# Optimization experiments

Measured on AMD Instinct MI355X. Metric: run time of the kernel, lower is better.

The kernel has to match this reference:

```python
import jax, jax.numpy as jnp
import numpy as np


def _next_fast_len(n):
    # smallest 5-smooth integer >= n (matches scipy.fftpack.next_fast_len)
    while True:
        m = n
        for p in (2, 3, 5):
            while m % p == 0:
                m //= p
        if m == 1:
            return n
        n += 1


def _conv1d_fft(values, weights):
    # values: [b, h, n, d], weights: [h, m]; FFT cross-correlation implementing
    # causal exponentially-decaying weighted sum (per-head EMA of values).
    N = values.shape[-2]
    M = weights.shape[-1]
    L = _next_fast_len(N + M - 1)
    f_v = jnp.fft.rfft(values, n=L, axis=-2)          # [b,h,F,d] complex
    f_w = jnp.fft.rfft(weights, n=L, axis=-1)         # [h,F]   complex
    out = jnp.fft.irfft(f_v * jnp.conj(f_w)[..., None], n=L, axis=-2)
    out = jnp.roll(out, -1, axis=-2)
    return out[..., L - N:, :]                         # [b,h,N,d]


def setup_inputs() -> dict:
    key = jax.random.key(0)
    ks = jax.random.split(key, 7)
    B, N, D, H = 4, 8192, 512, 8
    s = 1.0 / np.sqrt(D)
    return {
        "x": jax.random.normal(ks[0], (B, N, D), dtype=jnp.float32),
        "W_in": jax.random.normal(ks[1], (D, D), dtype=jnp.float32) * s,
        "b_in": jax.random.normal(ks[2], (D,), dtype=jnp.float32) * 0.01,
        "W_out": jax.random.normal(ks[3], (D, D), dtype=jnp.float32) * s,
        "b_out": jax.random.normal(ks[4], (D,), dtype=jnp.float32) * 0.01,
        "init_state": jax.random.normal(ks[5], (H, D // H), dtype=jnp.float32),
        "alpha_param": jax.random.normal(ks[6], (H,), dtype=jnp.float32),
    }


def reference(x, W_in, b_in, W_out, b_out, init_state, alpha_param):
    B, N, D = x.shape
    H, Dh = init_state.shape
    # input projection
    xp = x @ W_in.T + b_in                             # [B,N,D]
    xh = xp.reshape(B, N, H, Dh).transpose(0, 2, 1, 3)  # [B,H,N,Dh]
    # prepend learned init state, take first differences along time
    x0 = jnp.broadcast_to(init_state[None, :, None, :], (B, H, 1, Dh))
    xc = jnp.concatenate([x0, xh], axis=2)             # [B,H,N+1,Dh]
    xd = xc[:, :, 1:] - xc[:, :, :-1]                  # [B,H,N,Dh]
    # per-head smoothing coefficients
    alpha = jax.nn.sigmoid(alpha_param)[:, None]       # [H,1]
    ar = jnp.arange(N, dtype=x.dtype)
    weights = alpha * (1.0 - alpha) ** ar[::-1]        # [H,N]
    out = _conv1d_fft(xd, weights)                     # [B,H,N,Dh]
    # contribution of the initial state
    init_w = (1.0 - alpha) ** (ar + 1.0)               # [H,N]
    out = out + init_w[:, :, None] * init_state[:, None, :]
    out = out.transpose(0, 2, 1, 3).reshape(B, N, D)
    return out @ W_out.T + b_out
```

## Files before the change

kernel.cpp:

```cpp
#include <hip/hip_runtime.h>
#include <stdint.h>

#define SEQ      8192
#define BATCH    4
#define DIM      512
#define MROWS    32768
#define CHUNK    64
#define NCHUNK   128
#define NCHAN    2048

typedef unsigned short ushort;
typedef unsigned int   uint;
typedef __bf16 bf16x8 __attribute__((ext_vector_type(8)));
typedef float  f32x4  __attribute__((ext_vector_type(4)));
typedef ushort usx8   __attribute__((ext_vector_type(8)));

__device__ __forceinline__ ushort f2bf(float f) {
    unsigned u = __float_as_uint(f);
    unsigned r = (u + 0x7fffu + ((u >> 16) & 1u)) >> 16;
    return (ushort)r;
}
__device__ __forceinline__ float bf2f(ushort v) {
    return __uint_as_float(((unsigned)v) << 16);
}

__global__ void weights_to_bf16_kernel(const float* __restrict__ w_in,
                                       const float* __restrict__ w_out,
                                       ushort* __restrict__ dst, int n4each) {
    int i = blockIdx.x * blockDim.x + threadIdx.x;
    if (i >= 2 * n4each) return;
    const float4* src = (i < n4each) ? (const float4*)w_in
                                     : (const float4*)w_out - n4each;
    float4 v = src[i];
    ushort4 r;
    r.x = f2bf(v.x); r.y = f2bf(v.y); r.z = f2bf(v.z); r.w = f2bf(v.w);
    ((ushort4*)dst)[i] = r;
}

#define GLDS(g, l) __builtin_amdgcn_global_load_lds(                        \
        (const __attribute__((address_space(1))) void*)(g),                 \
        (__attribute__((address_space(3))) void*)(l), 16, 0, 0)

template <bool A_F32, bool OUT_BF16>
__global__ __launch_bounds__(512, 4) void gemm_kernel(
        const void* __restrict__ Aptr, const ushort* __restrict__ Bw,
        const float* __restrict__ bias, void* __restrict__ Cout,
        int M, int N, int K)
{
    __shared__ __align__(16) ushort As[2][128 * 32];
    __shared__ __align__(16) ushort Bs[2][256 * 32];

    const int tid  = threadIdx.x;
    const int lane = tid & 63;
    const int wave = tid >> 6;
    const int wr = wave >> 2, wc = wave & 3;
    const int bm = blockIdx.y, bn = blockIdx.x;
    const int quad = lane >> 4, r16 = lane & 15;

    const int srow = tid >> 2;
    const int skoff = (tid & 3) * 8;
    const float*  Ag32 = (const float*) Aptr + (size_t)(bm * 128 + srow) * K + skoff;
    const ushort* Ag16 = (const ushort*)Aptr + (size_t)(bm * 128 + srow) * K + skoff;
    const ushort* Bg0 = Bw + (size_t)(bn * 256 + srow) * K + skoff;
    const ushort* Bg1 = Bg0 + (size_t)128 * K;

    f32x4 acc[4][4];
    #pragma unroll
    for (int i = 0; i < 4; i++)
        #pragma unroll
        for (int j = 0; j < 4; j++)
            acc[i][j] = f32x4{0.f, 0.f, 0.f, 0.f};

    const int nIter = K / 32;

    auto stageB = [&](int k0, int b) {
        GLDS(Bg0 + k0, &Bs[b][tid * 8]);
        GLDS(Bg1 + k0, &Bs[b][128 * 32 + tid * 8]);
    };
    auto stageA16 = [&](int k0, int b) {
        GLDS(Ag16 + k0, &As[b][tid * 8]);
    };

    stageB(0, 0);
    float a0[8];
    if (A_F32) {
        #pragma unroll
        for (int u = 0; u < 8; u++) a0[u] = Ag32[u];
        usx8 w;
        #pragma unroll
        for (int u = 0; u < 8; u++) w[u] = f2bf(a0[u]);
        *(usx8*)&As[0][tid * 8] = w;
    } else {
        stageA16(0, 0);
    }

    int buf = 0;
    for (int k = 0; k < nIter; ++k) {
        __syncthreads();

        float anext[8];
        const bool more = (k + 1 < nIter);
        if (more) {
            const int ko = (k + 1) * 32;
            stageB(ko, buf ^ 1);
            if (A_F32) {
                #pragma unroll
                for (int u = 0; u < 8; u++) anext[u] = Ag32[ko + u];
            } else {
                stageA16(ko, buf ^ 1);
            }
        }

        bf16x8 af[4], bfr[4];
        #pragma unroll
        for (int i = 0; i < 4; i++)
            af[i] = *(const bf16x8*)&As[buf][(wr * 64 + i * 16 + r16) * 32 + quad * 8];
        #pragma unroll
        for (int j = 0; j < 4; j++)
            bfr[j] = *(const bf16x8*)&Bs[buf][(wc * 64 + j * 16 + r16) * 32 + quad * 8];

        #pragma unroll
        for (int i = 0; i < 4; i++)
            #pragma unroll
            for (int j = 0; j < 4; j++)
                acc[i][j] = __builtin_amdgcn_mfma_f32_16x16x32_bf16(
                                bfr[j], af[i], acc[i][j], 0, 0, 0);

        if (A_F32 && more) {
            usx8 w;
            #pragma unroll
            for (int u = 0; u < 8; u++) w[u] = f2bf(anext[u]);
            *(usx8*)&As[buf ^ 1][tid * 8] = w;
        }
        buf ^= 1;
    }

    #pragma unroll
    for (int i = 0; i < 4; i++) {
        const int m = bm * 128 + wr * 64 + i * 16 + r16;
        #pragma unroll
        for (int j = 0; j < 4; j++) {
            const int n0 = bn * 256 + wc * 64 + j * 16 + quad * 4;
            const float4 bv = *(const float4*)&bias[n0];
            float v0 = acc[i][j][0] + bv.x;
            float v1 = acc[i][j][1] + bv.y;
            float v2 = acc[i][j][2] + bv.z;
            float v3 = acc[i][j][3] + bv.w;
            size_t idx = (size_t)m * N + n0;
            if (OUT_BF16) {
                ushort4 r;
                r.x = f2bf(v0); r.y = f2bf(v1); r.z = f2bf(v2); r.w = f2bf(v3);
                *(ushort4*)&((ushort*)Cout)[idx] = r;
            } else {
                *(float4*)&((float*)Cout)[idx] = make_float4(v0, v1, v2, v3);
            }
        }
    }
}

template <bool WRITE_Z>
__global__ void scan_kernel(const ushort* __restrict__ xp,
                            const float* __restrict__ alpha_param,
                            const float* __restrict__ init_state,
                            const float* __restrict__ Zin,
                            float* __restrict__ Lfin,
                            ushort* __restrict__ zout)
{
    const int tid   = threadIdx.x;
    const int chunk = blockIdx.x;
    const int b     = blockIdx.y;
    const int d0    = tid * 2;
    const int h     = d0 >> 6;

    const float alpha = 1.0f / (1.0f + expf(-alpha_param[h]));
    const float cdec  = 1.0f - alpha;
    const int   t0    = chunk * CHUNK;
    const size_t baseRow = (size_t)b * SEQ;
    const int ch0 = b * DIM + d0;

    float prev0, prev1;
    if (chunk == 0) {
        prev0 = init_state[d0]; prev1 = init_state[d0 + 1];
    } else {
        uint u = *(const uint*)&xp[(baseRow + t0 - 1) * DIM + d0];
        prev0 = bf2f((ushort)(u & 0xffffu)); prev1 = bf2f((ushort)(u >> 16));
    }
    float z0 = 0.f, z1 = 0.f;
    if (WRITE_Z) {
        z0 = Zin[(size_t)ch0 * NCHUNK + chunk];
        z1 = Zin[(size_t)(ch0 + 1) * NCHUNK + chunk];
    }

    const ushort* p = xp + (baseRow + t0) * DIM + d0;
    ushort* q = WRITE_Z ? (zout + (baseRow + t0) * DIM + d0) : nullptr;
    #pragma unroll 8
    for (int t = 0; t < CHUNK; ++t) {
        uint u = *(const uint*)&p[(size_t)t * DIM];
        float cur0 = bf2f((ushort)(u & 0xffffu));
        float cur1 = bf2f((ushort)(u >> 16));
        z0 = cdec * z0 + alpha * (cur0 - prev0);
        z1 = cdec * z1 + alpha * (cur1 - prev1);
        prev0 = cur0; prev1 = cur1;
        if (WRITE_Z) {
            uint w = (uint)f2bf(z0) | ((uint)f2bf(z1) << 16);
            *(uint*)&q[(size_t)t * DIM] = w;
        }
    }
    if (!WRITE_Z) {
        Lfin[(size_t)ch0 * NCHUNK + chunk]       = z0;
        Lfin[(size_t)(ch0 + 1) * NCHUNK + chunk] = z1;
    }
}

__global__ void scan_fix_kernel(const float* __restrict__ Lfin,
                                const float* __restrict__ alpha_param,
                                const float* __restrict__ init_state,
                                float* __restrict__ Zin)
{
    int ch = blockIdx.x * blockDim.x + threadIdx.x;
    if (ch >= NCHAN) return;
    int d = ch & (DIM - 1);
    int h = d >> 6;
    float alpha = 1.0f / (1.0f + expf(-alpha_param[h]));
    float c = 1.0f - alpha;
    float cT = c;
    #pragma unroll
    for (int i = 0; i < 6; i++) cT *= cT;
    float Z = init_state[d];
    const float* L = Lfin + (size_t)ch * NCHUNK;
    float*      Zp = Zin  + (size_t)ch * NCHUNK;
    for (int i = 0; i < NCHUNK; i++) { Zp[i] = Z; Z = L[i] + cT * Z; }
}

extern "C" void kernel_launch(void* const* d_in, const int* in_sizes, int n_in,
                              void* d_out, int out_size, void* d_ws, size_t ws_size,
                              hipStream_t stream) {
    const float* x           = (const float*)d_in[0];
    const float* W_in        = (const float*)d_in[1];
    const float* b_in        = (const float*)d_in[2];
    const float* W_out       = (const float*)d_in[3];
    const float* b_out       = (const float*)d_in[4];
    const float* init_state  = (const float*)d_in[5];
    const float* alpha_param = (const float*)d_in[6];
    float* out = (float*)d_out;

    ushort* z_bf    = (ushort*)d_ws;
    ushort* win_bf  = z_bf   + (size_t)MROWS * DIM;
    ushort* wout_bf = win_bf + (size_t)DIM * DIM;
    ushort* xp_bf   = wout_bf + (size_t)DIM * DIM;
    float*  Lfin    = (float*)(xp_bf + (size_t)MROWS * DIM);
    float*  Zin     = Lfin + (size_t)NCHAN * NCHUNK;

    const int nw4 = (DIM * DIM) / 4;
    weights_to_bf16_kernel<<<(2 * nw4 + 255) / 256, 256, 0, stream>>>(
        W_in, W_out, win_bf, nw4);

    dim3 ggrid(DIM / 256, MROWS / 128);
    gemm_kernel<true, true><<<ggrid, 512, 0, stream>>>(
        (const void*)x, win_bf, b_in, (void*)xp_bf, MROWS, DIM, DIM);

    dim3 sgrid(NCHUNK, BATCH);
    scan_kernel<false><<<sgrid, 256, 0, stream>>>(
        xp_bf, alpha_param, init_state, nullptr, Lfin, nullptr);
    scan_fix_kernel<<<NCHAN / 256, 256, 0, stream>>>(
        Lfin, alpha_param, init_state, Zin);
    scan_kernel<true><<<sgrid, 256, 0, stream>>>(
        xp_bf, alpha_param, init_state, Zin, nullptr, z_bf);

    gemm_kernel<false, false><<<ggrid, 512, 0, stream>>>(
        (const void*)z_bf, wout_bf, b_out, (void*)out, MROWS, DIM, DIM);
}
```

Measured before the change: 212.8 us.

## Fuse chunk carry-in correction into output GEMM, dropping second scan pass

The local scan now writes chunk-local EMA results straight to the z buffer and emits chunk-final states in a chunk-major layout. The carry fix-up kernel reads that transposed layout with register prefetching. The second full scan pass over xp is removed: the output GEMM's A-loader adds the (1-alpha)^(tau+1)·Zin carry term while staging each tile. This saves a full read of xp and a full write of z, at the cost of extra ALU and Zin loads in the GEMM loader. It also adds one more bf16 rounding of the corrected value.

```diff
diff --git a/kernel.cpp b/kernel.cpp
--- a/kernel.cpp
+++ b/kernel.cpp
@@ -8,6 +8,7 @@
 #define CHUNK    64
 #define NCHUNK   128
 #define NCHAN    2048
+#define NHEAD    8
 
 typedef unsigned short ushort;
 typedef unsigned int   uint;
@@ -41,10 +42,11 @@
         (const __attribute__((address_space(1))) void*)(g),                 \
         (__attribute__((address_space(3))) void*)(l), 16, 0, 0)
 
-template <bool A_F32, bool OUT_BF16>
+template <int AMODE, bool OUT_BF16>
 __global__ __launch_bounds__(512, 4) void gemm_kernel(
         const void* __restrict__ Aptr, const ushort* __restrict__ Bw,
         const float* __restrict__ bias, void* __restrict__ Cout,
+        const float* __restrict__ Zin, const float* __restrict__ alpha_param,
         int M, int N, int K)
 {
     __shared__ __align__(16) ushort As[2][128 * 32];
@@ -63,6 +65,54 @@
     const ushort* Ag16 = (const ushort*)Aptr + (size_t)(bm * 128 + srow) * K + skoff;
     const ushort* Bg0 = Bw + (size_t)(bn * 256 + srow) * K + skoff;
     const ushort* Bg1 = Bg0 + (size_t)128 * K;
+
+    float fc0=0.f,fc1=0.f,fc2=0.f,fc3=0.f,fc4=0.f,fc5=0.f,fc6=0.f,fc7=0.f;
+    const float* Zc = nullptr;
+    if (AMODE == 2) {
+        const int m   = bm * 128 + srow;
+        const int tau = m & (CHUNK - 1);
+        const int bb  = m >> 13;
+        const int tch = (m & (SEQ - 1)) >> 6;
+        Zc = Zin + (size_t)tch * NCHAN + (size_t)bb * DIM;
+        const float t1 = (float)(tau + 1);
+        float a, c;
+        a = 1.f/(1.f+expf(-alpha_param[0])); c = 1.f - a; fc0 = exp2f(t1 * log2f(c));
+        a = 1.f/(1.f+expf(-alpha_param[1])); c = 1.f - a; fc1 = exp2f(t1 * log2f(c));
+        a = 1.f/(1.f+expf(-alpha_param[2])); c = 1.f - a; fc2 = exp2f(t1 * log2f(c));
+        a = 1.f/(1.f+expf(-alpha_param[3])); c = 1.f - a; fc3 = exp2f(t1 * log2f(c));
+        a = 1.f/(1.f+expf(-alpha_param[4])); c = 1.f - a; fc4 = exp2f(t1 * log2f(c));
+        a = 1.f/(1.f+expf(-alpha_param[5])); c = 1.f - a; fc5 = exp2f(t1 * log2f(c));
+        a = 1.f/(1.f+expf(-alpha_param[6])); c = 1.f - a; fc6 = exp2f(t1 * log2f(c));
+        a = 1.f/(1.f+expf(-alpha_param[7])); c = 1.f - a; fc7 = exp2f(t1 * log2f(c));
+    }
+    auto selfac = [&](int hh) -> float {
+        float f = fc0;
+        f = (hh == 1) ? fc1 : f;
+        f = (hh == 2) ? fc2 : f;
+        f = (hh == 3) ? fc3 : f;
+        f = (hh == 4) ? fc4 : f;
+        f = (hh == 5) ? fc5 : f;
+        f = (hh == 6) ? fc6 : f;
+        f = (hh == 7) ? fc7 : f;
+        return f;
+    };
+    auto stageA2 = [&](int ko, int b) {
+        usx8 av = *(const usx8*)(Ag16 + ko);
+        const int dbase = ko + skoff;
+        float4 zv0 = *(const float4*)&Zc[dbase];
+        float4 zv1 = *(const float4*)&Zc[dbase + 4];
+        float fac = selfac(dbase >> 6);
+        usx8 w;
+        w[0] = f2bf(bf2f(av[0]) + fac * zv0.x);
+        w[1] = f2bf(bf2f(av[1]) + fac * zv0.y);
+        w[2] = f2bf(bf2f(av[2]) + fac * zv0.z);
+        w[3] = f2bf(bf2f(av[3]) + fac * zv0.w);
+        w[4] = f2bf(bf2f(av[4]) + fac * zv1.x);
+        w[5] = f2bf(bf2f(av[5]) + fac * zv1.y);
+        w[6] = f2bf(bf2f(av[6]) + fac * zv1.z);
+        w[7] = f2bf(bf2f(av[7]) + fac * zv1.w);
+        *(usx8*)&As[b][tid * 8] = w;
+    };
 
     f32x4 acc[4][4];
     #pragma unroll
@@ -82,14 +132,16 @@
     };
 
     stageB(0, 0);
-    float a0[8];
-    if (A_F32) {
+    if (AMODE == 1) {
+        float a0[8];
         #pragma unroll
         for (int u = 0; u < 8; u++) a0[u] = Ag32[u];
         usx8 w;
         #pragma unroll
         for (int u = 0; u < 8; u++) w[u] = f2bf(a0[u]);
         *(usx8*)&As[0][tid * 8] = w;
+    } else if (AMODE == 2) {
+        stageA2(0, 0);
     } else {
         stageA16(0, 0);
     }
@@ -99,13 +151,20 @@
         __syncthreads();
 
         float anext[8];
+        usx8 av_n; float4 zn0, zn1; float fac_n = 0.f;
         const bool more = (k + 1 < nIter);
         if (more) {
             const int ko = (k + 1) * 32;
             stageB(ko, buf ^ 1);
-            if (A_F32) {
+            if (AMODE == 1) {
                 #pragma unroll
                 for (int u = 0; u < 8; u++) anext[u] = Ag32[ko + u];
+            } else if (AMODE == 2) {
+                av_n = *(const usx8*)(Ag16 + ko);
+                const int dbase = ko + skoff;
+                zn0 = *(const float4*)&Zc[dbase];
+                zn1 = *(const float4*)&Zc[dbase + 4];
+                fac_n = selfac(dbase >> 6);
             } else {
                 stageA16(ko, buf ^ 1);
             }
@@ -126,11 +185,24 @@
                 acc[i][j] = __builtin_amdgcn_mfma_f32_16x16x32_bf16(
                                 bfr[j], af[i], acc[i][j], 0, 0, 0);
 
-        if (A_F32 && more) {
-            usx8 w;
-            #pragma unroll
-            for (int u = 0; u < 8; u++) w[u] = f2bf(anext[u]);
-            *(usx8*)&As[buf ^ 1][tid * 8] = w;
+        if (more) {
+            if (AMODE == 1) {
+                usx8 w;
+                #pragma unroll
+                for (int u = 0; u < 8; u++) w[u] = f2bf(anext[u]);
+                *(usx8*)&As[buf ^ 1][tid * 8] = w;
+            } else if (AMODE == 2) {
+                usx8 w;
+                w[0] = f2bf(bf2f(av_n[0]) + fac_n * zn0.x);
+                w[1] = f2bf(bf2f(av_n[1]) + fac_n * zn0.y);
+                w[2] = f2bf(bf2f(av_n[2]) + fac_n * zn0.z);
+                w[3] = f2bf(bf2f(av_n[3]) + fac_n * zn0.w);
+                w[4] = f2bf(bf2f(av_n[4]) + fac_n * zn1.x);
+                w[5] = f2bf(bf2f(av_n[5]) + fac_n * zn1.y);
+                w[6] = f2bf(bf2f(av_n[6]) + fac_n * zn1.z);
+                w[7] = f2bf(bf2f(av_n[7]) + fac_n * zn1.w);
+                *(usx8*)&As[buf ^ 1][tid * 8] = w;
+            }
         }
         buf ^= 1;
     }
@@ -158,13 +230,11 @@
     }
 }
 
-template <bool WRITE_Z>
-__global__ void scan_kernel(const ushort* __restrict__ xp,
-                            const float* __restrict__ alpha_param,
-                            const float* __restrict__ init_state,
-                            const float* __restrict__ Zin,
-                            float* __restrict__ Lfin,
-                            ushort* __restrict__ zout)
+__global__ void scan_local_kernel(const ushort* __restrict__ xp,
+                                  const float* __restrict__ alpha_param,
+                                  const float* __restrict__ init_state,
+                                  float* __restrict__ Lfin,
+                                  ushort* __restrict__ zout)
 {
     const int tid   = threadIdx.x;
     const int chunk = blockIdx.x;
@@ -186,13 +256,8 @@
         prev0 = bf2f((ushort)(u & 0xffffu)); prev1 = bf2f((ushort)(u >> 16));
     }
     float z0 = 0.f, z1 = 0.f;
-    if (WRITE_Z) {
-        z0 = Zin[(size_t)ch0 * NCHUNK + chunk];
-        z1 = Zin[(size_t)(ch0 + 1) * NCHUNK + chunk];
-    }
-
-    const ushort* p = xp + (baseRow + t0) * DIM + d0;
-    ushort* q = WRITE_Z ? (zout + (baseRow + t0) * DIM + d0) : nullptr;
+    const ushort* p = xp   + (baseRow + t0) * DIM + d0;
+    ushort*       q = zout + (baseRow + t0) * DIM + d0;
     #pragma unroll 8
     for (int t = 0; t < CHUNK; ++t) {
         uint u = *(const uint*)&p[(size_t)t * DIM];
@@ -201,21 +266,16 @@
         z0 = cdec * z0 + alpha * (cur0 - prev0);
         z1 = cdec * z1 + alpha * (cur1 - prev1);
         prev0 = cur0; prev1 = cur1;
-        if (WRITE_Z) {
-            uint w = (uint)f2bf(z0) | ((uint)f2bf(z1) << 16);
-            *(uint*)&q[(size_t)t * DIM] = w;
-        }
-    }
-    if (!WRITE_Z) {
-        Lfin[(size_t)ch0 * NCHUNK + chunk]       = z0;
-        Lfin[(size_t)(ch0 + 1) * NCHUNK + chunk] = z1;
-    }
-}
-
-__global__ void scan_fix_kernel(const float* __restrict__ Lfin,
-                                const float* __restrict__ alpha_param,
-                                const float* __restrict__ init_state,
-                                float* __restrict__ Zin)
+        uint w = (uint)f2bf(z0) | ((uint)f2bf(z1) << 16);
+        *(uint*)&q[(size_t)t * DIM] = w;
+    }
+    *(float2*)&Lfin[(size_t)chunk * NCHAN + ch0] = make_float2(z0, z1);
+}
+
+__global__ void scan_fix2_kernel(const float* __restrict__ Lfin,
+                                 const float* __restrict__ alpha_param,
+                                 const float* __restrict__ init_state,
+                                 float* __restrict__ Zin)
 {
     int ch = blockIdx.x * blockDim.x + threadIdx.x;
     if (ch >= NCHAN) return;
@@ -227,9 +287,22 @@
     #pragma unroll
     for (int i = 0; i < 6; i++) cT *= cT;
     float Z = init_state[d];
-    const float* L = Lfin + (size_t)ch * NCHUNK;
-    float*      Zp = Zin  + (size_t)ch * NCHUNK;
-    for (int i = 0; i < NCHUNK; i++) { Zp[i] = Z; Z = L[i] + cT * Z; }
+    const float* Lp = Lfin + ch;
+    float*       Zp = Zin  + ch;
+    constexpr int PF = 16;
+    float Lr[PF];
+    #pragma unroll
+    for (int j = 0; j < PF; ++j) Lr[j] = Lp[(size_t)j * NCHAN];
+    for (int g = 0; g < NCHUNK / PF; ++g) {
+        #pragma unroll
+        for (int j = 0; j < PF; ++j) {
+            float Lc = Lr[j];
+            if (g + 1 < NCHUNK / PF)
+                Lr[j] = Lp[(size_t)((g + 1) * PF + j) * NCHAN];
+            Zp[(size_t)(g * PF + j) * NCHAN] = Z;
+            Z = Lc + cT * Z;
+        }
+    }
 }
 
 extern "C" void kernel_launch(void* const* d_in, const int* in_sizes, int n_in,
@@ -256,17 +329,17 @@
         W_in, W_out, win_bf, nw4);
 
     dim3 ggrid(DIM / 256, MROWS / 128);
-    gemm_kernel<true, true><<<ggrid, 512, 0, stream>>>(
-        (const void*)x, win_bf, b_in, (void*)xp_bf, MROWS, DIM, DIM);
+    gemm_kernel<1, true><<<ggrid, 512, 0, stream>>>(
+        (const void*)x, win_bf, b_in, (void*)xp_bf,
+        nullptr, nullptr, MROWS, DIM, DIM);
 
     dim3 sgrid(NCHUNK, BATCH);
-    scan_kernel<false><<<sgrid, 256, 0, stream>>>(
-        xp_bf, alpha_param, init_state, nullptr, Lfin, nullptr);
-    scan_fix_kernel<<<NCHAN / 256, 256, 0, stream>>>(
+    scan_local_kernel<<<sgrid, 256, 0, stream>>>(
+        xp_bf, alpha_param, init_state, Lfin, z_bf);
+    scan_fix2_kernel<<<NCHAN / 256, 256, 0, stream>>>(
         Lfin, alpha_param, init_state, Zin);
-    scan_kernel<true><<<sgrid, 256, 0, stream>>>(
-        xp_bf, alpha_param, init_state, Zin, nullptr, z_bf);
-
-    gemm_kernel<false, false><<<ggrid, 512, 0, stream>>>(
-        (const void*)z_bf, wout_bf, b_out, (void*)out, MROWS, DIM, DIM);
-}
+
+    gemm_kernel<2, false><<<ggrid, 512, 0, stream>>>(
+        (const void*)z_bf, wout_bf, b_out, (void*)out,
+        Zin, alpha_param, MROWS, DIM, DIM);
+}
```

Result: faster. 208.5 us (-2.0%).

## Fuse input GEMM with chunk-local scan and apply carry correction in output GEMM

Applied to the files above, without the earlier changes.

The input projection GEMM now runs the per-chunk EMA scan in its epilogue from a shared-memory tile. It writes chunk-local z and chunk summaries directly, which removes the xp round trip through global memory and both scan passes. A small fix-up kernel computes per-chunk carries. The output GEMM folds the decayed carry into its A operand as it loads it into shared memory. W_in is converted to bf16 inline, and W_out conversion is packed into extra blocks of the first kernel. The cost is extra in-loop f32 conversion and pow work in the GEMMs, and z is rounded to bf16 before the correction is added.

```diff
diff --git a/kernel.cpp b/kernel.cpp
--- a/kernel.cpp
+++ b/kernel.cpp
@@ -8,6 +8,9 @@
 #define CHUNK    64
 #define NCHUNK   128
 #define NCHAN    2048
+#define NHEAD    8
+#define NGCHUNK  512
+#define XLD      264
 
 typedef unsigned short ushort;
 typedef unsigned int   uint;
@@ -24,28 +27,206 @@
     return __uint_as_float(((unsigned)v) << 16);
 }
 
-__global__ void weights_to_bf16_kernel(const float* __restrict__ w_in,
-                                       const float* __restrict__ w_out,
-                                       ushort* __restrict__ dst, int n4each) {
-    int i = blockIdx.x * blockDim.x + threadIdx.x;
-    if (i >= 2 * n4each) return;
-    const float4* src = (i < n4each) ? (const float4*)w_in
-                                     : (const float4*)w_out - n4each;
-    float4 v = src[i];
-    ushort4 r;
-    r.x = f2bf(v.x); r.y = f2bf(v.y); r.z = f2bf(v.z); r.w = f2bf(v.w);
-    ((ushort4*)dst)[i] = r;
+__global__ __launch_bounds__(512, 4) void gemm1_scan_kernel(
+        const float* __restrict__ x,    const float* __restrict__ W_in,
+        const float* __restrict__ b_in, const float* __restrict__ W_out,
+        const float* __restrict__ alpha_param,
+        ushort* __restrict__ zout,      ushort* __restrict__ wout_bf,
+        float* __restrict__ Lfin,       float* __restrict__ XpT)
+{
+    const int tid = threadIdx.x;
+    const int bn  = blockIdx.x;
+
+    if (blockIdx.y == 0) {
+        const float4* src = (const float4*)W_out;
+        const int n4 = (DIM * DIM) / 4;
+        for (int idx = bn * 512 + tid; idx < n4; idx += 1024) {
+            float4 v = src[idx];
+            ushort4 r;
+            r.x = f2bf(v.x); r.y = f2bf(v.y); r.z = f2bf(v.z); r.w = f2bf(v.w);
+            ((ushort4*)wout_bf)[idx] = r;
+        }
+        return;
+    }
+    const int bm = blockIdx.y - 1;
+
+    __shared__ __align__(16) char smem[2 * XLD * 128];
+    ushort* As0 = (ushort*)smem;
+    ushort* Bs0 = (ushort*)(smem + 16384);
+    ushort* X   = (ushort*)smem;
+
+    const int lane = tid & 63;
+    const int wave = tid >> 6;
+    const int wr = wave >> 2, wc = wave & 3;
+    const int quad = lane >> 4, r16 = lane & 15;
+
+    const int srow  = tid >> 2;
+    const int skoff = (tid & 3) * 8;
+    const float* Ag  = x    + (size_t)(bm * 128 + srow) * DIM + skoff;
+    const float* Bg0 = W_in + (size_t)(bn * 256 + srow) * DIM + skoff;
+    const float* Bg1 = Bg0  + (size_t)128 * DIM;
+
+    f32x4 acc[4][4];
+    #pragma unroll
+    for (int i = 0; i < 4; i++)
+        #pragma unroll
+        for (int j = 0; j < 4; j++)
+            acc[i][j] = f32x4{0.f, 0.f, 0.f, 0.f};
+
+    const int nIter = DIM / 32;
+
+    auto cvt8 = [&](const float* s) {
+        usx8 w;
+        #pragma unroll
+        for (int u = 0; u < 8; u++) w[u] = f2bf(s[u]);
+        return w;
+    };
+
+    {
+        float a[8], b0[8], b1[8];
+        #pragma unroll
+        for (int u = 0; u < 8; u++) { a[u] = Ag[u]; b0[u] = Bg0[u]; b1[u] = Bg1[u]; }
+        *(usx8*)&As0[tid * 8]        = cvt8(a);
+        *(usx8*)&Bs0[tid * 8]        = cvt8(b0);
+        *(usx8*)&Bs0[4096 + tid * 8] = cvt8(b1);
+    }
+
+    int buf = 0;
+    for (int k = 0; k < nIter; ++k) {
+        __syncthreads();
+
+        float an[8], bn0[8], bn1[8];
+        const bool more = (k + 1 < nIter);
+        if (more) {
+            const int ko = (k + 1) * 32;
+            #pragma unroll
+            for (int u = 0; u < 8; u++) {
+                an[u]  = Ag[ko + u];
+                bn0[u] = Bg0[ko + u];
+                bn1[u] = Bg1[ko + u];
+            }
+        }
+
+        bf16x8 af[4], bfr[4];
+        #pragma unroll
+        for (int i = 0; i < 4; i++)
+            af[i] = *(const bf16x8*)&As0[buf * 4096 + (wr * 64 + i * 16 + r16) * 32 + quad * 8];
+        #pragma unroll
+        for (int j = 0; j < 4; j++)
+            bfr[j] = *(const bf16x8*)&Bs0[buf * 8192 + (wc * 64 + j * 16 + r16) * 32 + quad * 8];
+
+        #pragma unroll
+        for (int i = 0; i < 4; i++)
+            #pragma unroll
+            for (int j = 0; j < 4; j++)
+                acc[i][j] = __builtin_amdgcn_mfma_f32_16x16x32_bf16(
+                                bfr[j], af[i], acc[i][j], 0, 0, 0);
+
+        if (more) {
+            const int nb = buf ^ 1;
+            *(usx8*)&As0[nb * 4096 + tid * 8]        = cvt8(an);
+            *(usx8*)&Bs0[nb * 8192 + tid * 8]        = cvt8(bn0);
+            *(usx8*)&Bs0[nb * 8192 + 4096 + tid * 8] = cvt8(bn1);
+        }
+        buf ^= 1;
+    }
+
+    __syncthreads();
+    #pragma unroll
+    for (int i = 0; i < 4; i++) {
+        const int ml = wr * 64 + i * 16 + r16;
+        #pragma unroll
+        for (int j = 0; j < 4; j++) {
+            const int nl = wc * 64 + j * 16 + quad * 4;
+            const float4 bv = *(const float4*)&b_in[bn * 256 + nl];
+            ushort4 r4;
+            r4.x = f2bf(acc[i][j][0] + bv.x);
+            r4.y = f2bf(acc[i][j][1] + bv.y);
+            r4.z = f2bf(acc[i][j][2] + bv.z);
+            r4.w = f2bf(acc[i][j][3] + bv.w);
+            *(ushort4*)&X[ml * XLD + nl] = r4;
+        }
+    }
+    __syncthreads();
+
+    const int chalf = tid >> 8;
+    const int cidx  = tid & 255;
+    const int g     = 2 * bm + chalf;
+    const int d     = bn * 256 + cidx;
+    const int h     = d >> 6;
+    const float alpha = 1.0f / (1.0f + expf(-alpha_param[h]));
+    const float c     = 1.0f - alpha;
+
+    const ushort* Xr  = X + chalf * 64 * XLD + cidx;
+    ushort* zrow = zout + ((size_t)(bm * 128 + chalf * 64)) * DIM + d;
+
+    float z = 0.f, prev = 0.f;
+    #pragma unroll 8
+    for (int r = 0; r < CHUNK; ++r) {
+        float xv = bf2f(Xr[r * XLD]);
+        z = c * z + alpha * (xv - prev);
+        prev = xv;
+        zrow[(size_t)r * DIM] = f2bf(z);
+    }
+    Lfin[(size_t)g * 512 + d]       = z;
+    XpT[(size_t)(g + 1) * 512 + d]  = prev;
+}
+
+__global__ void scan_fixg_kernel(const float* __restrict__ Lfin,
+                                 const float* __restrict__ XpT,
+                                 const float* __restrict__ alpha_param,
+                                 const float* __restrict__ init_state,
+                                 float* __restrict__ G)
+{
+    int ch = blockIdx.x * blockDim.x + threadIdx.x;
+    if (ch >= NCHAN) return;
+    const int b = ch >> 9;
+    const int d = ch & (DIM - 1);
+    const int h = d >> 6;
+    const float alpha = 1.0f / (1.0f + expf(-alpha_param[h]));
+    const float c = 1.0f - alpha;
+    const float c2 = c * c, c4 = c2 * c2, c8 = c4 * c4,
+                c16 = c8 * c8, c32 = c16 * c16;
+    const float c63 = c32 * c16 * c8 * c4 * c2 * c;
+    const float sinit = init_state[d];
+
+    float Z = sinit;
+    const float* Lp = Lfin + (size_t)(b * NCHUNK) * 512 + d;
+    const float* Xp = XpT  + (size_t)(b * NCHUNK) * 512 + d;
+    float*       Gp = G    + (size_t)(b * NCHUNK) * 512 + d;
+
+    constexpr int PF = 16;
+    float Lr[PF], Xr[PF];
+    #pragma unroll
+    for (int j = 0; j < PF; ++j) {
+        Lr[j] = Lp[(size_t)j * 512];
+        Xr[j] = Xp[(size_t)j * 512];
+    }
+    for (int gr = 0; gr < NCHUNK / PF; ++gr) {
+        #pragma unroll
+        for (int j = 0; j < PF; ++j) {
+            const int kl = gr * PF + j;
+            const float xpt = (kl == 0) ? sinit : Xr[j];
+            const float Lc  = Lr[j];
+            if (gr + 1 < NCHUNK / PF) {
+                Lr[j] = Lp[(size_t)((gr + 1) * PF + j) * 512];
+                Xr[j] = Xp[(size_t)((gr + 1) * PF + j) * 512];
+            }
+            const float Gv = c * Z - alpha * xpt;
+            Gp[(size_t)kl * 512] = Gv;
+            Z = Lc + c63 * Gv;
+        }
+    }
 }
 
 #define GLDS(g, l) __builtin_amdgcn_global_load_lds(                        \
         (const __attribute__((address_space(1))) void*)(g),                 \
         (__attribute__((address_space(3))) void*)(l), 16, 0, 0)
 
-template <bool A_F32, bool OUT_BF16>
-__global__ __launch_bounds__(512, 4) void gemm_kernel(
-        const void* __restrict__ Aptr, const ushort* __restrict__ Bw,
-        const float* __restrict__ bias, void* __restrict__ Cout,
-        int M, int N, int K)
+__global__ __launch_bounds__(512, 4) void gemm2_kernel(
+        const ushort* __restrict__ Az, const ushort* __restrict__ Bw,
+        const float* __restrict__ bias, float* __restrict__ Cout,
+        const float* __restrict__ G, const float* __restrict__ alpha_param)
 {
     __shared__ __align__(16) ushort As[2][128 * 32];
     __shared__ __align__(16) ushort Bs[2][256 * 32];
@@ -57,12 +238,51 @@
     const int bm = blockIdx.y, bn = blockIdx.x;
     const int quad = lane >> 4, r16 = lane & 15;
 
-    const int srow = tid >> 2;
+    const int srow  = tid >> 2;
     const int skoff = (tid & 3) * 8;
-    const float*  Ag32 = (const float*) Aptr + (size_t)(bm * 128 + srow) * K + skoff;
-    const ushort* Ag16 = (const ushort*)Aptr + (size_t)(bm * 128 + srow) * K + skoff;
-    const ushort* Bg0 = Bw + (size_t)(bn * 256 + srow) * K + skoff;
-    const ushort* Bg1 = Bg0 + (size_t)128 * K;
+    const ushort* Ag16 = Az + (size_t)(bm * 128 + srow) * DIM + skoff;
+    const ushort* Bg0  = Bw + (size_t)(bn * 256 + srow) * DIM + skoff;
+    const ushort* Bg1  = Bg0 + (size_t)128 * DIM;
+
+    const int m   = bm * 128 + srow;
+    const int tau = m & (CHUNK - 1);
+    const float* Gc = G + (size_t)(m >> 6) * 512;
+    const float t1 = (float)tau;
+    float fc0,fc1,fc2,fc3,fc4,fc5,fc6,fc7;
+    {
+        float a, c;
+        a = 1.f/(1.f+expf(-alpha_param[0])); c = 1.f - a; fc0 = exp2f(t1 * log2f(c));
+        a = 1.f/(1.f+expf(-alpha_param[1])); c = 1.f - a; fc1 = exp2f(t1 * log2f(c));
+        a = 1.f/(1.f+expf(-alpha_param[2])); c = 1.f - a; fc2 = exp2f(t1 * log2f(c));
+        a = 1.f/(1.f+expf(-alpha_param[3])); c = 1.f - a; fc3 = exp2f(t1 * log2f(c));
+        a = 1.f/(1.f+expf(-alpha_param[4])); c = 1.f - a; fc4 = exp2f(t1 * log2f(c));
+        a = 1.f/(1.f+expf(-alpha_param[5])); c = 1.f - a; fc5 = exp2f(t1 * log2f(c));
+        a = 1.f/(1.f+expf(-alpha_param[6])); c = 1.f - a; fc6 = exp2f(t1 * log2f(c));
+        a = 1.f/(1.f+expf(-alpha_param[7])); c = 1.f - a; fc7 = exp2f(t1 * log2f(c));
+    }
+    auto selfac = [&](int hh) -> float {
+        float f = fc0;
+        f = (hh == 1) ? fc1 : f;
+        f = (hh == 2) ? fc2 : f;
+        f = (hh == 3) ? fc3 : f;
+        f = (hh == 4) ? fc4 : f;
+        f = (hh == 5) ? fc5 : f;
+        f = (hh == 6) ? fc6 : f;
+        f = (hh == 7) ? fc7 : f;
+        return f;
+    };
+    auto fixpack = [&](usx8 av, float4 z0, float4 z1, float fac) {
+        usx8 w;
+        w[0] = f2bf(bf2f(av[0]) + fac * z0.x);
+        w[1] = f2bf(bf2f(av[1]) + fac * z0.y);
+        w[2] = f2bf(bf2f(av[2]) + fac * z0.z);
+        w[3] = f2bf(bf2f(av[3]) + fac * z0.w);
+        w[4] = f2bf(bf2f(av[4]) + fac * z1.x);
+        w[5] = f2bf(bf2f(av[5]) + fac * z1.y);
+        w[6] = f2bf(bf2f(av[6]) + fac * z1.z);
+        w[7] = f2bf(bf2f(av[7]) + fac * z1.w);
+        return w;
+    };
 
     f32x4 acc[4][4];
     #pragma unroll
@@ -71,44 +291,35 @@
         for (int j = 0; j < 4; j++)
             acc[i][j] = f32x4{0.f, 0.f, 0.f, 0.f};
 
-    const int nIter = K / 32;
+    const int nIter = DIM / 32;
 
     auto stageB = [&](int k0, int b) {
         GLDS(Bg0 + k0, &Bs[b][tid * 8]);
         GLDS(Bg1 + k0, &Bs[b][128 * 32 + tid * 8]);
     };
-    auto stageA16 = [&](int k0, int b) {
-        GLDS(Ag16 + k0, &As[b][tid * 8]);
-    };
 
     stageB(0, 0);
-    float a0[8];
-    if (A_F32) {
-        #pragma unroll
-        for (int u = 0; u < 8; u++) a0[u] = Ag32[u];
-        usx8 w;
-        #pragma unroll
-        for (int u = 0; u < 8; u++) w[u] = f2bf(a0[u]);
-        *(usx8*)&As[0][tid * 8] = w;
-    } else {
-        stageA16(0, 0);
+    {
+        usx8 av = *(const usx8*)(Ag16);
+        float4 z0 = *(const float4*)&Gc[skoff];
+        float4 z1 = *(const float4*)&Gc[skoff + 4];
+        *(usx8*)&As[0][tid * 8] = fixpack(av, z0, z1, selfac(skoff >> 6));
     }
 
     int buf = 0;
     for (int k = 0; k < nIter; ++k) {
         __syncthreads();
 
-        float anext[8];
+        usx8 av_n; float4 zn0, zn1; float fac_n = 0.f;
         const bool more = (k + 1 < nIter);
         if (more) {
             const int ko = (k + 1) * 32;
             stageB(ko, buf ^ 1);
-            if (A_F32) {
-                #pragma unroll
-                for (int u = 0; u < 8; u++) anext[u] = Ag32[ko + u];
-            } else {
-                stageA16(ko, buf ^ 1);
-            }
+            av_n = *(const usx8*)(Ag16 + ko);
+            const int dbase = ko + skoff;
+            zn0 = *(const float4*)&Gc[dbase];
+            zn1 = *(const float4*)&Gc[dbase + 4];
+            fac_n = selfac(dbase >> 6);
         }
 
         bf16x8 af[4], bfr[4];
@@ -126,110 +337,23 @@
                 acc[i][j] = __builtin_amdgcn_mfma_f32_16x16x32_bf16(
                                 bfr[j], af[i], acc[i][j], 0, 0, 0);
 
-        if (A_F32 && more) {
-            usx8 w;
-            #pragma unroll
-            for (int u = 0; u < 8; u++) w[u] = f2bf(anext[u]);
-            *(usx8*)&As[buf ^ 1][tid * 8] = w;
-        }
+        if (more)
+            *(usx8*)&As[buf ^ 1][tid * 8] = fixpack(av_n, zn0, zn1, fac_n);
         buf ^= 1;
     }
 
     #pragma unroll
     for (int i = 0; i < 4; i++) {
-        const int m = bm * 128 + wr * 64 + i * 16 + r16;
+        const int mr = bm * 128 + wr * 64 + i * 16 + r16;
         #pragma unroll
         for (int j = 0; j < 4; j++) {
             const int n0 = bn * 256 + wc * 64 + j * 16 + quad * 4;
             const float4 bv = *(const float4*)&bias[n0];
-            float v0 = acc[i][j][0] + bv.x;
-            float v1 = acc[i][j][1] + bv.y;
-            float v2 = acc[i][j][2] + bv.z;
-            float v3 = acc[i][j][3] + bv.w;
-            size_t idx = (size_t)m * N + n0;
-            if (OUT_BF16) {
-                ushort4 r;
-                r.x = f2bf(v0); r.y = f2bf(v1); r.z = f2bf(v2); r.w = f2bf(v3);
-                *(ushort4*)&((ushort*)Cout)[idx] = r;
-            } else {
-                *(float4*)&((float*)Cout)[idx] = make_float4(v0, v1, v2, v3);
-            }
-        }
-    }
-}
-
-template <bool WRITE_Z>
-__global__ void scan_kernel(const ushort* __restrict__ xp,
-                            const float* __restrict__ alpha_param,
-                            const float* __restrict__ init_state,
-                            const float* __restrict__ Zin,
-                            float* __restrict__ Lfin,
-                            ushort* __restrict__ zout)
-{
-    const int tid   = threadIdx.x;
-    const int chunk = blockIdx.x;
-    const int b     = blockIdx.y;
-    const int d0    = tid * 2;
-    const int h     = d0 >> 6;
-
-    const float alpha = 1.0f / (1.0f + expf(-alpha_param[h]));
-    const float cdec  = 1.0f - alpha;
-    const int   t0    = chunk * CHUNK;
-    const size_t baseRow = (size_t)b * SEQ;
-    const int ch0 = b * DIM + d0;
-
-    float prev0, prev1;
-    if (chunk == 0) {
-        prev0 = init_state[d0]; prev1 = init_state[d0 + 1];
-    } else {
-        uint u = *(const uint*)&xp[(baseRow + t0 - 1) * DIM + d0];
-        prev0 = bf2f((ushort)(u & 0xffffu)); prev1 = bf2f((ushort)(u >> 16));
-    }
-    float z0 = 0.f, z1 = 0.f;
-    if (WRITE_Z) {
-        z0 = Zin[(size_t)ch0 * NCHUNK + chunk];
-        z1 = Zin[(size_t)(ch0 + 1) * NCHUNK + chunk];
-    }
-
-    const ushort* p = xp + (baseRow + t0) * DIM + d0;
-    ushort* q = WRITE_Z ? (zout + (baseRow + t0) * DIM + d0) : nullptr;
-    #pragma unroll 8
-    for (int t = 0; t < CHUNK; ++t) {
-        uint u = *(const uint*)&p[(size_t)t * DIM];
-        float cur0 = bf2f((ushort)(u & 0xffffu));
-        float cur1 = bf2f((ushort)(u >> 16));
-        z0 = cdec * z0 + alpha * (cur0 - prev0);
-        z1 = cdec * z1 + alpha * (cur1 - prev1);
-        prev0 = cur0; prev1 = cur1;
-        if (WRITE_Z) {
-            uint w = (uint)f2bf(z0) | ((uint)f2bf(z1) << 16);
-            *(uint*)&q[(size_t)t * DIM] = w;
-        }
-    }
-    if (!WRITE_Z) {
-        Lfin[(size_t)ch0 * NCHUNK + chunk]       = z0;
-        Lfin[(size_t)(ch0 + 1) * NCHUNK + chunk] = z1;
-    }
-}
-
-__global__ void scan_fix_kernel(const float* __restrict__ Lfin,
-                                const float* __restrict__ alpha_param,
-                                const float* __restrict__ init_state,
-                                float* __restrict__ Zin)
-{
-    int ch = blockIdx.x * blockDim.x + threadIdx.x;
-    if (ch >= NCHAN) return;
-    int d = ch & (DIM - 1);
-    int h = d >> 6;
-    float alpha = 1.0f / (1.0f + expf(-alpha_param[h]));
-    float c = 1.0f - alpha;
-    float cT = c;
-    #pragma unroll
-    for (int i = 0; i < 6; i++) cT *= cT;
-    float Z = init_state[d];
-    const float* L = Lfin + (size_t)ch * NCHUNK;
-    float*      Zp = Zin  + (size_t)ch * NCHUNK;
-    for (int i = 0; i < NCHUNK; i++) { Zp[i] = Z; Z = L[i] + cT * Z; }
+            float4 v = make_float4(acc[i][j][0] + bv.x, acc[i][j][1] + bv.y,
+                                   acc[i][j][2] + bv.z, acc[i][j][3] + bv.w);
+            *(float4*)&Cout[(size_t)mr * DIM + n0] = v;
+        }
+    }
 }
 
 extern "C" void kernel_launch(void* const* d_in, const int* in_sizes, int n_in,
@@ -245,28 +369,19 @@
     float* out = (float*)d_out;
 
     ushort* z_bf    = (ushort*)d_ws;
-    ushort* win_bf  = z_bf   + (size_t)MROWS * DIM;
-    ushort* wout_bf = win_bf + (size_t)DIM * DIM;
-    ushort* xp_bf   = wout_bf + (size_t)DIM * DIM;
-    float*  Lfin    = (float*)(xp_bf + (size_t)MROWS * DIM);
-    float*  Zin     = Lfin + (size_t)NCHAN * NCHUNK;
-
-    const int nw4 = (DIM * DIM) / 4;
-    weights_to_bf16_kernel<<<(2 * nw4 + 255) / 256, 256, 0, stream>>>(
-        W_in, W_out, win_bf, nw4);
-
-    dim3 ggrid(DIM / 256, MROWS / 128);
-    gemm_kernel<true, true><<<ggrid, 512, 0, stream>>>(
-        (const void*)x, win_bf, b_in, (void*)xp_bf, MROWS, DIM, DIM);
-
-    dim3 sgrid(NCHUNK, BATCH);
-    scan_kernel<false><<<sgrid, 256, 0, stream>>>(
-        xp_bf, alpha_param, init_state, nullptr, Lfin, nullptr);
-    scan_fix_kernel<<<NCHAN / 256, 256, 0, stream>>>(
-        Lfin, alpha_param, init_state, Zin);
-    scan_kernel<true><<<sgrid, 256, 0, stream>>>(
-        xp_bf, alpha_param, init_state, Zin, nullptr, z_bf);
-
-    gemm_kernel<false, false><<<ggrid, 512, 0, stream>>>(
-        (const void*)z_bf, wout_bf, b_out, (void*)out, MROWS, DIM, DIM);
-}
+    ushort* wout_bf = z_bf + (size_t)MROWS * DIM;
+    float*  Lfin    = (float*)(wout_bf + (size_t)DIM * DIM);
+    float*  XpT     = Lfin + (size_t)NGCHUNK * 512;
+    float*  G       = XpT  + (size_t)(NGCHUNK + 1) * 512;
+
+    dim3 g1(2, MROWS / 128 + 1);
+    gemm1_scan_kernel<<<g1, 512, 0, stream>>>(
+        x, W_in, b_in, W_out, alpha_param, z_bf, wout_bf, Lfin, XpT);
+
+    scan_fixg_kernel<<<NCHAN / 256, 256, 0, stream>>>(
+        Lfin, XpT, alpha_param, init_state, G);
+
+    dim3 g2(2, MROWS / 128);
+    gemm2_kernel<<<g2, 512, 0, stream>>>(
+        z_bf, wout_bf, b_out, out, G, alpha_param);
+}
```

Result: faster. 202.0 us (-5.1%).
